# Optimization experiments

Measured on AMD Instinct MI355X. Metric: run time of the kernel, lower is better.

## Reference

```python
import jax, jax.numpy as jnp
import numpy as np

D_MODEL = 2048
N_HEADS = 16
N_KV = 4
GROUP = N_HEADS // N_KV  # 4
D_K = D_MODEL // N_HEADS  # 128
D_V = D_MODEL // N_KV     # 512
THETA = 10000.0
Q_DIM = N_HEADS * D_K
K_DIM = N_KV * D_K
V_DIM = N_KV * D_V


def _apply_rope(t, sin, cos):
    # t: [B, H, L, D]; sin/cos: [L, D] broadcast over batch/heads
    half = t.shape[-1] // 2
    x1, x2 = t[..., :half], t[..., half:]
    rot = jnp.concatenate([-x2, x1], axis=-1)
    return t * cos + rot * sin


def setup_inputs() -> dict:
    key = jax.random.key(0)
    k1, k2, k3 = jax.random.split(key, 3)
    x = jax.random.normal(k1, (2, 2048, D_MODEL), dtype=jnp.float32)
    # attn_proj: Linear(d_model -> Q_DIM+K_DIM+V_DIM, bias=False); stored as [in, out]
    W_attn = jax.random.normal(k2, (D_MODEL, Q_DIM + K_DIM + V_DIM), dtype=jnp.float32) * 0.02
    # out_proj: Linear(n_heads*d_v -> d_model) with bias
    W_out = jax.random.normal(k3, (N_HEADS * D_V, D_MODEL), dtype=jnp.float32) * 0.02
    b_out = jnp.zeros((D_MODEL,), dtype=jnp.float32)
    return {"x": x, "W_attn": W_attn, "W_out": W_out, "b_out": b_out}


def reference(x, W_attn, W_out, b_out):
    B, L, _ = x.shape
    qkv = x @ W_attn  # [B, L, Q_DIM+K_DIM+V_DIM]
    q = qkv[..., :Q_DIM].reshape(B, L, N_HEADS, D_K).transpose(0, 2, 1, 3)          # [B,H,L,dk]
    k = qkv[..., Q_DIM:Q_DIM + K_DIM].reshape(B, L, N_KV, D_K).transpose(0, 2, 1, 3)  # [B,Hkv,L,dk]
    v = qkv[..., Q_DIM + K_DIM:].reshape(B, L, N_KV, D_V).transpose(0, 2, 1, 3)       # [B,Hkv,L,dv]

    # RoPE (computed in float32, as in source)
    inv_freq = 1.0 / (THETA ** (jnp.arange(0, D_K, 2, dtype=jnp.float32) / D_K))
    freqs = jnp.arange(L, dtype=jnp.float32)[:, None] * inv_freq[None, :]  # [L, dk/2]
    ang = jnp.concatenate([freqs, freqs], axis=-1)                          # [L, dk]
    sin, cos = jnp.sin(ang), jnp.cos(ang)
    q = _apply_rope(q.astype(jnp.float32), sin, cos).astype(x.dtype)
    k = _apply_rope(k.astype(jnp.float32), sin, cos).astype(x.dtype)

    # GQA: repeat_interleave(group, dim=1) is equivalent to grouping q heads as [kv, group]
    qg = q.reshape(B, N_KV, GROUP, L, D_K)
    scores = jnp.einsum('bkgqd,bkld->bkgql', qg, k) / (D_K ** 0.5)  # [B,Hkv,G,L,L]
    probs = jax.nn.softmax(scores, axis=-1)
    ctx = jnp.einsum('bkgql,bkle->bkgqe', probs, v)  # [B,Hkv,G,L,dv]
    ctx = ctx.reshape(B, N_HEADS, L, D_V).transpose(0, 2, 1, 3).reshape(B, L, N_HEADS * D_V)
    return ctx @ W_out + b_out
```

## Files before the change

### kernel.cpp

```cpp
#include <hip/hip_runtime.h>

typedef unsigned short u16;
typedef float f32x4 __attribute__((ext_vector_type(4)));
typedef __bf16 bf16x8 __attribute__((ext_vector_type(8)));

#define DEV static __device__ __forceinline__

DEV u16 f2bf(float f) {
  union { float f; unsigned u; } c; c.f = f;
  unsigned u = c.u;
  u += 0x7fffu + ((u >> 16) & 1u);
  return (u16)(u >> 16);
}
DEV float bf2f(u16 h) {
  union { float f; unsigned u; } c; c.u = ((unsigned)h) << 16;
  return c.f;
}
DEV f32x4 MFMA(bf16x8 a, bf16x8 b, f32x4 c) {
  return __builtin_amdgcn_mfma_f32_16x16x32_bf16(a, b, c, 0, 0, 0);
}
DEV unsigned cvt_pk_bf16(float a, float b) {
  unsigned r;
  asm("v_cvt_pk_bf16_f32 %0, %1, %2" : "=v"(r) : "v"(a), "v"(b));
  return r;
}
DEV float ex2(float x) { return __builtin_amdgcn_exp2f(x); }
DEV void glds16(const void* src, void* lds) {
  __builtin_amdgcn_global_load_lds(
      (__attribute__((address_space(1))) void*)src,
      (__attribute__((address_space(3))) void*)lds, 16, 0, 0);
}
DEV void barrier_raw() {
  __builtin_amdgcn_sched_barrier(0);
  asm volatile("s_barrier" ::: "memory");
  __builtin_amdgcn_sched_barrier(0);
}
#define VMCNT(N)                                              \
  do {                                                        \
    asm volatile("s_waitcnt vmcnt(" #N ")" ::: "memory");     \
    __builtin_amdgcn_sched_barrier(0);                        \
  } while (0)


__global__ void prep_kernel(const float* __restrict__ x, const float* __restrict__ W_attn,
                            float* __restrict__ sinT, float* __restrict__ cosT,
                            u16* __restrict__ xb, u16* __restrict__ WbT) {
  __shared__ u16 tile[32][33];
  const int bk = blockIdx.x, t = threadIdx.x;
  if (bk < 512) {
    int idx = bk * 256 + t;
    int l = idx >> 6, i = idx & 63;
    float inv = __expf(-((float)(2 * i) / 128.0f) * 9.210340371976184f);
    float ang = (float)l * inv;
    sinT[idx] = sinf(ang);
    cosT[idx] = cosf(ang);
  } else if (bk < 8704) {
    int i = ((bk - 512) * 256 + t) * 4;
    float4 v = *(const float4*)(x + i);
    ushort4 o;
    o.x = f2bf(v.x); o.y = f2bf(v.y); o.z = f2bf(v.z); o.w = f2bf(v.w);
    *(ushort4*)(xb + i) = o;
  } else {
    int idx = bk - 8704;
    int c0 = (idx % 144) * 32, r0 = (idx / 144) * 32;
    int tx = t & 31, ty = t >> 5;
    for (int i = 0; i < 32; i += 8)
      tile[ty + i][tx] = f2bf(W_attn[(size_t)(r0 + ty + i) * 4608 + c0 + tx]);
    __syncthreads();
    for (int i = 0; i < 32; i += 8)
      WbT[(size_t)(c0 + ty + i) * 2048 + r0 + tx] = tile[tx][ty + i];
  }
}

__global__ void transpose_cast(const float* __restrict__ in, u16* __restrict__ out,
                               int R, int C) {
  __shared__ u16 tile[32][33];
  int c0 = blockIdx.x * 32, r0 = blockIdx.y * 32;
  int tx = threadIdx.x, ty = threadIdx.y;
  for (int i = 0; i < 32; i += 8)
    tile[ty + i][tx] = f2bf(in[(size_t)(r0 + ty + i) * C + c0 + tx]);
  __syncthreads();
  for (int i = 0; i < 32; i += 8)
    out[(size_t)(c0 + ty + i) * R + r0 + tx] = tile[tx][ty + i];
}

__global__ __launch_bounds__(512) void gemm1_8ph(const u16* __restrict__ A,
                                                 const u16* __restrict__ Bt,
                                                 u16* __restrict__ C) {
  constexpr int K = 2048, N = 4608, NT = 32;
  __shared__ __align__(16) u16 lA[2][2][8192];
  __shared__ __align__(16) u16 lB[2][2][8192];
  const int t = threadIdx.x, w = t >> 6, l = t & 63;
  const int lr = l & 15, lg = l >> 4;
  const int wr = w >> 2, wn = w & 3;
  const int swz = (blockIdx.x & 7) * 36 + (blockIdx.x >> 3);
  const int bm = swz & 15, bn = swz >> 4;

  const size_t aBase = (size_t)(bm * 256) * K;
  const size_t bBase = (size_t)(bn * 256) * K;
  const int lslog = (t & 3) ^ ((t >> 3) & 3);
  const int r128 = t >> 2;
  const int aswz = (lg ^ ((lr >> 1) & 3)) << 4;

  auto stA = [&](int buf, int kk, int tile) {
#pragma unroll
    for (int i = 0; i < 2; ++i) {
      int row = i * 128 + r128;
      glds16(A + aBase + (size_t)row * K + tile * 64 + kk * 32 + lslog * 8,
             &lA[buf][kk][i * 4096 + t * 8]);
    }
  };
  auto stB = [&](int buf, int kk, int tile) {
#pragma unroll
    for (int i = 0; i < 2; ++i) {
      int row = i * 128 + r128;
      glds16(Bt + bBase + (size_t)row * K + tile * 64 + kk * 32 + lslog * 8,
             &lB[buf][kk][i * 4096 + t * 8]);
    }
  };

  f32x4 acc[8][4];
#pragma unroll
  for (int f = 0; f < 8; ++f)
#pragma unroll
    for (int g = 0; g < 4; ++g) acc[f][g] = f32x4{0.f, 0.f, 0.f, 0.f};

  stA(0, 0, 0); stB(0, 0, 0); stA(0, 1, 0); stB(0, 1, 0); stA(1, 0, 1); stB(1, 0, 1);
  VMCNT(8);
  barrier_raw();

  auto PH = [&](int buf, int kk, int mh, auto&& st) {
    bf16x8 af[4], bb[4];
    const char* pA = (const char*)lA[buf][kk];
    const char* pB = (const char*)lB[buf][kk];
#pragma unroll
    for (int f = 0; f < 4; ++f) {
      af[f] = *(const bf16x8*)(pA + (wr * 128 + (mh * 4 + f) * 16 + lr) * 64 + aswz);
      bb[f] = *(const bf16x8*)(pB + (wn * 64 + f * 16 + lr) * 64 + aswz);
    }
    st();
    __builtin_amdgcn_s_setprio(1);
#pragma unroll
    for (int f = 0; f < 4; ++f)
#pragma unroll
      for (int g = 0; g < 4; ++g)
        acc[mh * 4 + f][g] = MFMA(af[f], bb[g], acc[mh * 4 + f][g]);
    __builtin_amdgcn_s_setprio(0);
  };
  auto NOST = [] {};

  for (int i = 0; i < NT / 2 - 1; ++i) {
    const int t1 = 2 * i + 1, t2 = 2 * i + 2, t3 = 2 * i + 3;
    PH(0, 0, 0, [&] { stA(1, 1, t1); });            barrier_raw();
    PH(0, 0, 1, [&] { stB(1, 1, t1); }); VMCNT(8);  barrier_raw();
    PH(0, 1, 0, [&] { stA(0, 0, t2); });            barrier_raw();
    PH(0, 1, 1, [&] { stB(0, 0, t2); }); VMCNT(8);  barrier_raw();
    PH(1, 0, 0, [&] { stA(0, 1, t2); });            barrier_raw();
    PH(1, 0, 1, [&] { stB(0, 1, t2); }); VMCNT(8);  barrier_raw();
    PH(1, 1, 0, [&] { stA(1, 0, t3); });            barrier_raw();
    PH(1, 1, 1, [&] { stB(1, 0, t3); }); VMCNT(8);  barrier_raw();
  }
  PH(0, 0, 0, [&] { stA(1, 1, NT - 1); });           barrier_raw();
  PH(0, 0, 1, [&] { stB(1, 1, NT - 1); }); VMCNT(8); barrier_raw();
  PH(0, 1, 0, NOST);                                 barrier_raw();
  PH(0, 1, 1, NOST);                       VMCNT(4); barrier_raw();
  PH(1, 0, 0, NOST);                                 barrier_raw();
  PH(1, 0, 1, NOST);                       VMCNT(0); barrier_raw();
  PH(1, 1, 0, NOST);                                 barrier_raw();
  PH(1, 1, 1, NOST);

  const int crow0 = bm * 256 + wr * 128;
  const int ccol0 = bn * 256 + wn * 64;
#pragma unroll
  for (int f = 0; f < 8; ++f)
#pragma unroll
    for (int g = 0; g < 4; ++g)
#pragma unroll
      for (int j = 0; j < 4; ++j)
        C[(size_t)(crow0 + f * 16 + lg * 4 + j) * N + ccol0 + g * 16 + lr] =
            f2bf(acc[f][g][j]);
}

__global__ __launch_bounds__(512) void gemm2_4ph(const u16* __restrict__ A,
                                                 const u16* __restrict__ Bt,
                                                 float* __restrict__ Cf,
                                                 const float* __restrict__ bias) {
  constexpr int K = 8192, N = 2048, NT = 128;
  __shared__ __align__(16) u16 lA[2][2][8192];
  __shared__ __align__(16) u16 lB[2][2][4096];
  const int t = threadIdx.x, w = t >> 6, l = t & 63;
  const int lr = l & 15, lg = l >> 4;
  const int wr = w >> 1, wn = w & 1;
  const int swz = (blockIdx.x & 7) * 32 + (blockIdx.x >> 3);
  const int bm = swz & 15, bn = swz >> 4;

  const size_t aBase = (size_t)(bm * 256) * K;
  const size_t bBase = (size_t)(bn * 128) * K;
  const int lslog = (t & 3) ^ ((t >> 3) & 3);
  const int r128 = t >> 2;
  const int aswz = (lg ^ ((lr >> 1) & 3)) << 4;

  auto stA = [&](int buf, int kk, int tile) {
#pragma unroll
    for (int i = 0; i < 2; ++i) {
      int row = i * 128 + r128;
      glds16(A + aBase + (size_t)row * K + tile * 64 + kk * 32 + lslog * 8,
             &lA[buf][kk][i * 4096 + t * 8]);
    }
  };
  auto stB = [&](int buf, int kk, int tile) {
    glds16(Bt + bBase + (size_t)r128 * K + tile * 64 + kk * 32 + lslog * 8,
           &lB[buf][kk][t * 8]);
  };

  f32x4 acc[4][4];
#pragma unroll
  for (int f = 0; f < 4; ++f)
#pragma unroll
    for (int g = 0; g < 4; ++g) acc[f][g] = f32x4{0.f, 0.f, 0.f, 0.f};

  stA(0, 0, 0); stB(0, 0, 0); stA(0, 1, 0); stB(0, 1, 0); stA(1, 0, 1); stB(1, 0, 1);
  VMCNT(6);
  barrier_raw();

  auto PH = [&](int buf, int kk, auto&& st) {
    bf16x8 af[4], bb[4];
    const char* pA = (const char*)lA[buf][kk];
    const char* pB = (const char*)lB[buf][kk];
#pragma unroll
    for (int f = 0; f < 4; ++f) {
      af[f] = *(const bf16x8*)(pA + (wr * 64 + f * 16 + lr) * 64 + aswz);
      bb[f] = *(const bf16x8*)(pB + (wn * 64 + f * 16 + lr) * 64 + aswz);
    }
    st();
    __builtin_amdgcn_s_setprio(1);
#pragma unroll
    for (int f = 0; f < 4; ++f)
#pragma unroll
      for (int g = 0; g < 4; ++g)
        acc[f][g] = MFMA(af[f], bb[g], acc[f][g]);
    __builtin_amdgcn_s_setprio(0);
  };
  auto NOST = [] {};

  for (int i = 0; i < NT / 2 - 1; ++i) {
    const int t1 = 2 * i + 1, t2 = 2 * i + 2, t3 = 2 * i + 3;
    PH(0, 0, [&] { stA(1, 1, t1); stB(1, 1, t1); }); VMCNT(6); barrier_raw();
    PH(0, 1, [&] { stA(0, 0, t2); stB(0, 0, t2); }); VMCNT(6); barrier_raw();
    PH(1, 0, [&] { stA(0, 1, t2); stB(0, 1, t2); }); VMCNT(6); barrier_raw();
    PH(1, 1, [&] { stA(1, 0, t3); stB(1, 0, t3); }); VMCNT(6); barrier_raw();
  }
  PH(0, 0, [&] { stA(1, 1, NT - 1); stB(1, 1, NT - 1); }); VMCNT(6); barrier_raw();
  PH(0, 1, NOST);                                          VMCNT(3); barrier_raw();
  PH(1, 0, NOST);                                          VMCNT(0); barrier_raw();
  PH(1, 1, NOST);

  const int crow0 = bm * 256 + wr * 64;
  const int ccol0 = bn * 128 + wn * 64;
#pragma unroll
  for (int g = 0; g < 4; ++g) {
    float bv = bias[ccol0 + g * 16 + lr];
#pragma unroll
    for (int f = 0; f < 4; ++f)
#pragma unroll
      for (int j = 0; j < 4; ++j)
        Cf[(size_t)(crow0 + f * 16 + lg * 4 + j) * N + ccol0 + g * 16 + lr] =
            acc[f][g][j] + bv;
  }
}

__global__ void ropevt_kernel(u16* __restrict__ qkv, const float* __restrict__ sinT,
                              const float* __restrict__ cosT, u16* __restrict__ vT) {
  __shared__ u16 tile[32][33];
  const int bk = blockIdx.x, t = threadIdx.x;
  if (bk < 20480) {
    int idx = bk * 256 + t;
    int d = idx & 63;
    int rh = idx >> 6;
    int head = rh % 20;
    int row = rh / 20;
    int lpos = row & 2047;
    int col = head < 16 ? head * 128 : 2048 + (head - 16) * 128;
    float sc = head < 16 ? 0.12751743561938476f : 1.0f;
    u16* p = qkv + (size_t)row * 4608 + col;
    float x1 = bf2f(p[d]), x2 = bf2f(p[d + 64]);
    float c = cosT[lpos * 64 + d], s = sinT[lpos * 64 + d];
    p[d]      = f2bf((x1 * c - x2 * s) * sc);
    p[d + 64] = f2bf((x2 * c + x1 * s) * sc);
  } else {
    int idx = bk - 20480;
    int bx = idx & 15, by = (idx >> 4) & 63, bkv = idx >> 10;
    int b = bkv >> 2, kv = bkv & 3;
    int e0 = bx * 32, l0 = by * 32;
    const u16* src = qkv + (size_t)(b * 2048) * 4608 + 2560 + kv * 512;
    int tx = t & 31, ty = t >> 5;
    for (int i = 0; i < 32; i += 8)
      tile[ty + i][tx] = src[(size_t)(l0 + ty + i) * 4608 + e0 + tx];
    __syncthreads();
    u16* dst = vT + (size_t)(bkv * 512) * 2048;
    int pi = ((tx >> 2) & 3) * 8 + ((tx >> 4) & 1) * 4 + (tx & 3);
    for (int i = 0; i < 32; i += 8)
      dst[(size_t)(e0 + ty + i) * 2048 + l0 + pi] = tile[tx][ty + i];
  }
}

__global__ __launch_bounds__(512, 2) void attn_kernel(
    const u16* __restrict__ qkv, const u16* __restrict__ vT,
    u16* __restrict__ ctxb) {
  const int wg = blockIdx.x;
  const int pg = wg & 7, qt = wg >> 3;
  const int kvg = pg & 3, b = pg >> 2;
  const int t = threadIdx.x, w = t >> 6, l = t & 63;
  const int lr = l & 15, lg = l >> 4;
  const int h4 = w >> 1, eh = w & 1;
  const int h = kvg * 4 + h4;

  __shared__ __align__(16) u16 lK[2][64 * 128];
  __shared__ __align__(16) u16 lV[2][512 * 64];

  f32x4 zero = {0.f, 0.f, 0.f, 0.f};

  bf16x8 qf[2][4];
  const size_t qbase = (size_t)(b * 2048 + qt * 32);
#pragma unroll
  for (int m = 0; m < 2; ++m)
#pragma unroll
    for (int dc = 0; dc < 4; ++dc)
      qf[m][dc] = *(const bf16x8*)(qkv + (qbase + m * 16 + lr) * 4608 + h * 128 + dc * 32 + lg * 8);

  f32x4 acc[2][16];
#pragma unroll
  for (int m = 0; m < 2; ++m)
#pragma unroll
    for (int e = 0; e < 16; ++e) acc[m][e] = zero;
  float m_r[2] = {-1e30f, -1e30f};
  float l_r[2] = {0.f, 0.f};

  const size_t kbase = (size_t)(b * 2048) * 4608 + 2048 + kvg * 128;
  const size_t vbase = (size_t)((b * 4 + kvg) * 512) * 2048;

  const int krow = t >> 4;
  const int kp = t & 15;
  const int ks = (kp & 8) | ((kp ^ (krow & 7)) & 7);
  const u16* ksrc0 = qkv + kbase + (size_t)krow * 4608 + ks * 8;
  const int vs = (t & 7) ^ ((t >> 3) & 7);
  const int ve0 = (t >> 3) * 2 + (vs >> 2);
  const u16* vsrc0 = vT + vbase + (size_t)ve0 * 2048 + (vs & 3) * 8;

  const int vfoff = (eh * 128 + (lr >> 1)) * 128 +
                    (((((lr & 1) << 2) | lg) ^ ((lr >> 1) & 7)) << 4);

  auto stage = [&](int bi, int kv0) {
#pragma unroll
    for (int i = 0; i < 2; ++i)
      glds16(ksrc0 + (size_t)(kv0 + i * 32) * 4608, &lK[bi][i * 4096 + t * 8]);
#pragma unroll
    for (int hh = 0; hh < 2; ++hh)
#pragma unroll
      for (int i = 0; i < 4; ++i)
        glds16(vsrc0 + (kv0 + hh * 32) + (size_t)i * 262144,
               &lV[bi][hh * 16384 + i * 4096 + t * 8]);
  };

  stage(0, 0);

  auto half_body = [&](const char* lKc, const char* lVc) {
    f32x4 sT[2][2];
    sT[0][0] = zero; sT[0][1] = zero; sT[1][0] = zero; sT[1][1] = zero;
    __builtin_amdgcn_s_setprio(1);
#pragma unroll
    for (int dc = 0; dc < 4; ++dc) {
      int slot = dc * 4 + lg;
      int sw = (slot & 8) | ((slot ^ (lr & 7)) & 7);
#pragma unroll
      for (int kt = 0; kt < 2; ++kt) {
        bf16x8 kf = *(const bf16x8*)(lKc + (kt * 16 + lr) * 256 + sw * 16);
        sT[kt][0] = MFMA(kf, qf[0][dc], sT[kt][0]);
        sT[kt][1] = MFMA(kf, qf[1][dc], sT[kt][1]);
      }
    }
    __builtin_amdgcn_s_setprio(0);

    float lmax[2];
#pragma unroll
    for (int m = 0; m < 2; ++m) {
      float a0 = fmaxf(fmaxf(sT[0][m][0], sT[0][m][1]), fmaxf(sT[0][m][2], sT[0][m][3]));
      float a1 = fmaxf(fmaxf(sT[1][m][0], sT[1][m][1]), fmaxf(sT[1][m][2], sT[1][m][3]));
      lmax[m] = fmaxf(a0, a1);
    }
    bool need = (lmax[0] > m_r[0] + 11.5f) || (lmax[1] > m_r[1] + 11.5f);
    if (__any(need)) {
#pragma unroll
      for (int m = 0; m < 2; ++m) {
        float r = lmax[m];
        r = fmaxf(r, __shfl_xor(r, 16));
        r = fmaxf(r, __shfl_xor(r, 32));
        float mn = fmaxf(m_r[m], r);
        float al = ex2(m_r[m] - mn);
        m_r[m] = mn; l_r[m] *= al;
        float alj[4];
#pragma unroll
        for (int j = 0; j < 4; ++j) alj[j] = __shfl(al, lg * 4 + j);
#pragma unroll
        for (int e = 0; e < 16; ++e)
#pragma unroll
          for (int j = 0; j < 4; ++j) acc[m][e][j] *= alj[j];
      }
    }

    bf16x8 pf[2];
#pragma unroll
    for (int m = 0; m < 2; ++m) {
      float p0 = ex2(sT[0][m][0] - m_r[m]), p1 = ex2(sT[0][m][1] - m_r[m]);
      float p2 = ex2(sT[0][m][2] - m_r[m]), p3 = ex2(sT[0][m][3] - m_r[m]);
      float p4 = ex2(sT[1][m][0] - m_r[m]), p5 = ex2(sT[1][m][1] - m_r[m]);
      float p6 = ex2(sT[1][m][2] - m_r[m]), p7 = ex2(sT[1][m][3] - m_r[m]);
      l_r[m] += ((p0 + p1) + (p2 + p3)) + ((p4 + p5) + (p6 + p7));
      union { bf16x8 v; unsigned wd[4]; } u;
      u.wd[0] = cvt_pk_bf16(p0, p1);
      u.wd[1] = cvt_pk_bf16(p2, p3);
      u.wd[2] = cvt_pk_bf16(p4, p5);
      u.wd[3] = cvt_pk_bf16(p6, p7);
      pf[m] = u.v;
    }

    __builtin_amdgcn_s_setprio(1);
#pragma unroll
    for (int e = 0; e < 16; ++e) {
      bf16x8 vf = *(const bf16x8*)(lVc + vfoff + e * 1024);
      acc[0][e] = MFMA(pf[0], vf, acc[0][e]);
      acc[1][e] = MFMA(pf[1], vf, acc[1][e]);
    }
    __builtin_amdgcn_s_setprio(0);
  };

  for (int it = 0; it < 32; ++it) {
    const int cur = it & 1;
    __syncthreads();
    if (it + 1 < 32) stage(cur ^ 1, 64 * (it + 1));
    const char* lKc = (const char*)lK[cur];
    const char* lVc = (const char*)lV[cur];
    half_body(lKc, lVc);
    half_body(lKc + 8192, lVc + 32768);
  }

#pragma unroll
  for (int m = 0; m < 2; ++m) {
    float s = l_r[m];
    s += __shfl_xor(s, 16);
    s += __shfl_xor(s, 32);
    l_r[m] = s;
  }
#pragma unroll
  for (int m = 0; m < 2; ++m) {
    float linv[4];
#pragma unroll
    for (int j = 0; j < 4; ++j) linv[j] = 1.0f / __shfl(l_r[m], lg * 4 + j);
    const size_t orow0 = qbase + m * 16 + lg * 4;
#pragma unroll
    for (int e = 0; e < 16; ++e)
#pragma unroll
      for (int j = 0; j < 4; ++j)
        ctxb[(orow0 + j) * 8192 + h * 512 + eh * 256 + e * 16 + lr] =
            f2bf(acc[m][e][j] * linv[j]);
  }
}

extern "C" void kernel_launch(void* const* d_in, const int* in_sizes, int n_in,
                              void* d_out, int out_size, void* d_ws, size_t ws_size,
                              hipStream_t stream) {
  const float* x      = (const float*)d_in[0];
  const float* W_attn = (const float*)d_in[1];
  const float* W_out  = (const float*)d_in[2];
  const float* b_out  = (const float*)d_in[3];
  float* out = (float*)d_out;
  char* ws = (char*)d_ws;

  if (ws_size < 158334976u) return;

  float* sinT = (float*)(ws + 0);
  float* cosT = (float*)(ws + 524288);
  u16* xb   = (u16*)(ws + 1048576);
  u16* WbT  = (u16*)(ws + 17825792);
  u16* qkvb = (u16*)(ws + 36700160);
  u16* vT   = (u16*)(ws + 74448896);
  u16* ctxb = (u16*)(ws + 91226112);
  u16* WobT = (u16*)(ws + 1048576);

  prep_kernel<<<17920, 256, 0, stream>>>(x, W_attn, sinT, cosT, xb, WbT);
  gemm1_8ph<<<288, 512, 0, stream>>>(xb, WbT, qkvb);
  ropevt_kernel<<<28672, 256, 0, stream>>>(qkvb, sinT, cosT, vT);
  attn_kernel<<<512, 512, 0, stream>>>(qkvb, vT, ctxb);
  transpose_cast<<<dim3(64, 256), dim3(32, 8), 0, stream>>>(W_out, WobT, 8192, 2048);
  gemm2_4ph<<<256, 512, 0, stream>>>(ctxb, WobT, out, b_out);
}
```

Measured before the change: 557.8 us.

## Unify GEMMs into templated 256x128 kernel and widen transpose-cast tiles to 64x64

Replaces the 256x256 8-phase QKV GEMM with a templated 256x128 4-phase GEMM shared with the output projection. The QKV GEMM now launches 576 blocks instead of 288, which should balance work across CUs better at the cost of more redundant loads of the A operand. The W_attn and W_out transpose-casts move to 64x64 tiles with float4 loads and ushort4 stores, aiming for wider memory transactions and fewer blocks.

```diff
diff --git a/kernel.cpp b/kernel.cpp
--- a/kernel.cpp
+++ b/kernel.cpp
@@ -45,7 +45,7 @@
 __global__ void prep_kernel(const float* __restrict__ x, const float* __restrict__ W_attn,
                             float* __restrict__ sinT, float* __restrict__ cosT,
                             u16* __restrict__ xb, u16* __restrict__ WbT) {
-  __shared__ u16 tile[32][33];
+  __shared__ u16 tile[64][72];
   const int bk = blockIdx.x, t = threadIdx.x;
   if (bk < 512) {
     int idx = bk * 256 + t;
@@ -62,136 +62,69 @@
     *(ushort4*)(xb + i) = o;
   } else {
     int idx = bk - 8704;
-    int c0 = (idx % 144) * 32, r0 = (idx / 144) * 32;
-    int tx = t & 31, ty = t >> 5;
-    for (int i = 0; i < 32; i += 8)
-      tile[ty + i][tx] = f2bf(W_attn[(size_t)(r0 + ty + i) * 4608 + c0 + tx]);
+    int c0 = (idx % 72) * 64, r0 = (idx / 72) * 64;
+    int tc = (t & 15) * 4, tr = t >> 4;
+#pragma unroll
+    for (int i = 0; i < 4; ++i) {
+      int r = tr + i * 16;
+      float4 v = *(const float4*)(W_attn + (size_t)(r0 + r) * 4608 + c0 + tc);
+      tile[tc + 0][r] = f2bf(v.x);
+      tile[tc + 1][r] = f2bf(v.y);
+      tile[tc + 2][r] = f2bf(v.z);
+      tile[tc + 3][r] = f2bf(v.w);
+    }
     __syncthreads();
-    for (int i = 0; i < 32; i += 8)
-      WbT[(size_t)(c0 + ty + i) * 2048 + r0 + tx] = tile[tx][ty + i];
-  }
-}
-
-__global__ void transpose_cast(const float* __restrict__ in, u16* __restrict__ out,
-                               int R, int C) {
-  __shared__ u16 tile[32][33];
-  int c0 = blockIdx.x * 32, r0 = blockIdx.y * 32;
-  int tx = threadIdx.x, ty = threadIdx.y;
-  for (int i = 0; i < 32; i += 8)
-    tile[ty + i][tx] = f2bf(in[(size_t)(r0 + ty + i) * C + c0 + tx]);
+#pragma unroll
+    for (int i = 0; i < 4; ++i) {
+      int cc = tr + i * 16;
+      ushort4 o;
+      o.x = tile[cc][tc]; o.y = tile[cc][tc + 1];
+      o.z = tile[cc][tc + 2]; o.w = tile[cc][tc + 3];
+      *(ushort4*)(WbT + (size_t)(c0 + cc) * 2048 + r0 + tc) = o;
+    }
+  }
+}
+
+__global__ void transpose_cast64(const float* __restrict__ in, u16* __restrict__ out,
+                                 int R, int C) {
+  __shared__ u16 tile[64][72];
+  int c0 = blockIdx.x * 64, r0 = blockIdx.y * 64;
+  int t = threadIdx.x;
+  int tc = (t & 15) * 4, tr = t >> 4;
+#pragma unroll
+  for (int i = 0; i < 4; ++i) {
+    int r = tr + i * 16;
+    float4 v = *(const float4*)(in + (size_t)(r0 + r) * C + c0 + tc);
+    tile[tc + 0][r] = f2bf(v.x);
+    tile[tc + 1][r] = f2bf(v.y);
+    tile[tc + 2][r] = f2bf(v.z);
+    tile[tc + 3][r] = f2bf(v.w);
+  }
   __syncthreads();
-  for (int i = 0; i < 32; i += 8)
-    out[(size_t)(c0 + ty + i) * R + r0 + tx] = tile[tx][ty + i];
-}
-
-__global__ __launch_bounds__(512) void gemm1_8ph(const u16* __restrict__ A,
-                                                 const u16* __restrict__ Bt,
-                                                 u16* __restrict__ C) {
-  constexpr int K = 2048, N = 4608, NT = 32;
-  __shared__ __align__(16) u16 lA[2][2][8192];
-  __shared__ __align__(16) u16 lB[2][2][8192];
-  const int t = threadIdx.x, w = t >> 6, l = t & 63;
-  const int lr = l & 15, lg = l >> 4;
-  const int wr = w >> 2, wn = w & 3;
-  const int swz = (blockIdx.x & 7) * 36 + (blockIdx.x >> 3);
-  const int bm = swz & 15, bn = swz >> 4;
-
-  const size_t aBase = (size_t)(bm * 256) * K;
-  const size_t bBase = (size_t)(bn * 256) * K;
-  const int lslog = (t & 3) ^ ((t >> 3) & 3);
-  const int r128 = t >> 2;
-  const int aswz = (lg ^ ((lr >> 1) & 3)) << 4;
-
-  auto stA = [&](int buf, int kk, int tile) {
-#pragma unroll
-    for (int i = 0; i < 2; ++i) {
-      int row = i * 128 + r128;
-      glds16(A + aBase + (size_t)row * K + tile * 64 + kk * 32 + lslog * 8,
-             &lA[buf][kk][i * 4096 + t * 8]);
-    }
-  };
-  auto stB = [&](int buf, int kk, int tile) {
-#pragma unroll
-    for (int i = 0; i < 2; ++i) {
-      int row = i * 128 + r128;
-      glds16(Bt + bBase + (size_t)row * K + tile * 64 + kk * 32 + lslog * 8,
-             &lB[buf][kk][i * 4096 + t * 8]);
-    }
-  };
-
-  f32x4 acc[8][4];
-#pragma unroll
-  for (int f = 0; f < 8; ++f)
-#pragma unroll
-    for (int g = 0; g < 4; ++g) acc[f][g] = f32x4{0.f, 0.f, 0.f, 0.f};
-
-  stA(0, 0, 0); stB(0, 0, 0); stA(0, 1, 0); stB(0, 1, 0); stA(1, 0, 1); stB(1, 0, 1);
-  VMCNT(8);
-  barrier_raw();
-
-  auto PH = [&](int buf, int kk, int mh, auto&& st) {
-    bf16x8 af[4], bb[4];
-    const char* pA = (const char*)lA[buf][kk];
-    const char* pB = (const char*)lB[buf][kk];
-#pragma unroll
-    for (int f = 0; f < 4; ++f) {
-      af[f] = *(const bf16x8*)(pA + (wr * 128 + (mh * 4 + f) * 16 + lr) * 64 + aswz);
-      bb[f] = *(const bf16x8*)(pB + (wn * 64 + f * 16 + lr) * 64 + aswz);
-    }
-    st();
-    __builtin_amdgcn_s_setprio(1);
-#pragma unroll
-    for (int f = 0; f < 4; ++f)
-#pragma unroll
-      for (int g = 0; g < 4; ++g)
-        acc[mh * 4 + f][g] = MFMA(af[f], bb[g], acc[mh * 4 + f][g]);
-    __builtin_amdgcn_s_setprio(0);
-  };
-  auto NOST = [] {};
-
-  for (int i = 0; i < NT / 2 - 1; ++i) {
-    const int t1 = 2 * i + 1, t2 = 2 * i + 2, t3 = 2 * i + 3;
-    PH(0, 0, 0, [&] { stA(1, 1, t1); });            barrier_raw();
-    PH(0, 0, 1, [&] { stB(1, 1, t1); }); VMCNT(8);  barrier_raw();
-    PH(0, 1, 0, [&] { stA(0, 0, t2); });            barrier_raw();
-    PH(0, 1, 1, [&] { stB(0, 0, t2); }); VMCNT(8);  barrier_raw();
-    PH(1, 0, 0, [&] { stA(0, 1, t2); });            barrier_raw();
-    PH(1, 0, 1, [&] { stB(0, 1, t2); }); VMCNT(8);  barrier_raw();
-    PH(1, 1, 0, [&] { stA(1, 0, t3); });            barrier_raw();
-    PH(1, 1, 1, [&] { stB(1, 0, t3); }); VMCNT(8);  barrier_raw();
-  }
-  PH(0, 0, 0, [&] { stA(1, 1, NT - 1); });           barrier_raw();
-  PH(0, 0, 1, [&] { stB(1, 1, NT - 1); }); VMCNT(8); barrier_raw();
-  PH(0, 1, 0, NOST);                                 barrier_raw();
-  PH(0, 1, 1, NOST);                       VMCNT(4); barrier_raw();
-  PH(1, 0, 0, NOST);                                 barrier_raw();
-  PH(1, 0, 1, NOST);                       VMCNT(0); barrier_raw();
-  PH(1, 1, 0, NOST);                                 barrier_raw();
-  PH(1, 1, 1, NOST);
-
-  const int crow0 = bm * 256 + wr * 128;
-  const int ccol0 = bn * 256 + wn * 64;
-#pragma unroll
-  for (int f = 0; f < 8; ++f)
-#pragma unroll
-    for (int g = 0; g < 4; ++g)
-#pragma unroll
-      for (int j = 0; j < 4; ++j)
-        C[(size_t)(crow0 + f * 16 + lg * 4 + j) * N + ccol0 + g * 16 + lr] =
-            f2bf(acc[f][g][j]);
-}
-
-__global__ __launch_bounds__(512) void gemm2_4ph(const u16* __restrict__ A,
-                                                 const u16* __restrict__ Bt,
-                                                 float* __restrict__ Cf,
-                                                 const float* __restrict__ bias) {
-  constexpr int K = 8192, N = 2048, NT = 128;
+#pragma unroll
+  for (int i = 0; i < 4; ++i) {
+    int cc = tr + i * 16;
+    ushort4 o;
+    o.x = tile[cc][tc]; o.y = tile[cc][tc + 1];
+    o.z = tile[cc][tc + 2]; o.w = tile[cc][tc + 3];
+    *(ushort4*)(out + (size_t)(c0 + cc) * R + r0 + tc) = o;
+  }
+}
+
+template <int WRITE_F32, int K, int N>
+__global__ __launch_bounds__(512) void gemm_4ph(const u16* __restrict__ A,
+                                                const u16* __restrict__ Bt,
+                                                u16* __restrict__ Cb,
+                                                float* __restrict__ Cf,
+                                                const float* __restrict__ bias) {
+  constexpr int NT = K / 64;
+  constexpr int NBN = N / 128;
   __shared__ __align__(16) u16 lA[2][2][8192];
   __shared__ __align__(16) u16 lB[2][2][4096];
   const int t = threadIdx.x, w = t >> 6, l = t & 63;
   const int lr = l & 15, lg = l >> 4;
   const int wr = w >> 1, wn = w & 1;
-  const int swz = (blockIdx.x & 7) * 32 + (blockIdx.x >> 3);
+  const int swz = (blockIdx.x & 7) * (2 * NBN) + (blockIdx.x >> 3);
   const int bm = swz & 15, bn = swz >> 4;
 
   const size_t aBase = (size_t)(bm * 256) * K;
@@ -259,13 +192,15 @@
   const int ccol0 = bn * 128 + wn * 64;
 #pragma unroll
   for (int g = 0; g < 4; ++g) {
-    float bv = bias[ccol0 + g * 16 + lr];
+    float bv = WRITE_F32 ? bias[ccol0 + g * 16 + lr] : 0.f;
 #pragma unroll
     for (int f = 0; f < 4; ++f)
 #pragma unroll
-      for (int j = 0; j < 4; ++j)
-        Cf[(size_t)(crow0 + f * 16 + lg * 4 + j) * N + ccol0 + g * 16 + lr] =
-            acc[f][g][j] + bv;
+      for (int j = 0; j < 4; ++j) {
+        size_t off = (size_t)(crow0 + f * 16 + lg * 4 + j) * N + ccol0 + g * 16 + lr;
+        if (WRITE_F32) Cf[off] = acc[f][g][j] + bv;
+        else           Cb[off] = f2bf(acc[f][g][j]);
+      }
   }
 }
 
@@ -487,10 +422,10 @@
   u16* ctxb = (u16*)(ws + 91226112);
   u16* WobT = (u16*)(ws + 1048576);
 
-  prep_kernel<<<17920, 256, 0, stream>>>(x, W_attn, sinT, cosT, xb, WbT);
-  gemm1_8ph<<<288, 512, 0, stream>>>(xb, WbT, qkvb);
+  prep_kernel<<<11008, 256, 0, stream>>>(x, W_attn, sinT, cosT, xb, WbT);
+  gemm_4ph<0, 2048, 4608><<<576, 512, 0, stream>>>(xb, WbT, qkvb, nullptr, nullptr);
   ropevt_kernel<<<28672, 256, 0, stream>>>(qkvb, sinT, cosT, vT);
   attn_kernel<<<512, 512, 0, stream>>>(qkvb, vT, ctxb);
-  transpose_cast<<<dim3(64, 256), dim3(32, 8), 0, stream>>>(W_out, WobT, 8192, 2048);
-  gemm2_4ph<<<256, 512, 0, stream>>>(ctxb, WobT, out, b_out);
-}
+  transpose_cast64<<<dim3(32, 128), 256, 0, stream>>>(W_out, WobT, 8192, 2048);
+  gemm_4ph<1, 8192, 2048><<<256, 512, 0, stream>>>(ctxb, WobT, nullptr, out, b_out);
+}
```

Result: slower. 577.4 us (+3.5%).
